# Kernel tuning notes

Measured on AMD Instinct MI355X. Metric: run time of the kernel, lower is better.

## Reference

```python
import jax, jax.numpy as jnp
import numpy as np

B, T, C = 4, 2048, 1024
HEAD = 64  # n_embd // n_heads


def setup_inputs() -> dict:
    key = jax.random.key(0)
    kx, kk, kq, kv = jax.random.split(key, 4)
    x = jax.random.normal(kx, (B, T, C), dtype=jnp.float32)
    # nn.Linear(n_embd, head_size, bias=False) weights have shape [head_size, n_embd]
    s = 1.0 / np.sqrt(C)
    Wk = jax.random.normal(kk, (HEAD, C), dtype=jnp.float32) * s
    Wq = jax.random.normal(kq, (HEAD, C), dtype=jnp.float32) * s
    Wv = jax.random.normal(kv, (HEAD, C), dtype=jnp.float32) * s
    return {"x": x, "Wk": Wk, "Wq": Wq, "Wv": Wv}


def reference(x, Wk, Wq, Wv):
    Bx, Tx, Cx = x.shape
    k = jnp.einsum("btc,hc->bth", x, Wk)  # [B,T,HEAD]
    q = jnp.einsum("btc,hc->bth", x, Wq)
    v = jnp.einsum("btc,hc->bth", x, Wv)
    # NOTE: original scales by C**-0.5 (C = n_embd), not head_size**-0.5
    scale = Cx ** (-0.5)
    wei = jnp.einsum("bth,bsh->bts", q, k) * scale  # [B,T,T]
    causal = jnp.tril(jnp.ones((Tx, Tx), dtype=bool))
    wei = jnp.where(causal, wei, -jnp.inf)
    wei = jax.nn.softmax(wei, axis=-1)
    # dropout p=0.0 (eval) -> identity
    out = jnp.einsum("bts,bsh->bth", wei, v)  # [B,T,HEAD]
    return out
```

## Files before the change

kernel.cpp:

```cpp
#include <hip/hip_runtime.h>
#include <math.h>

#define Tn 2048
#define Cn 1024
#define Hn 64

using u16 = unsigned short;
typedef float f32x4 __attribute__((ext_vector_type(4)));
typedef __bf16 bf16x8 __attribute__((ext_vector_type(8)));
typedef u16 u16x8 __attribute__((ext_vector_type(8)));
typedef u16 u16x4 __attribute__((ext_vector_type(4)));

__device__ __forceinline__ u16 f2bf(float f) {
    return __builtin_bit_cast(u16, static_cast<__bf16>(f));
}

__global__ __launch_bounds__(256) void wpack_kernel(
    const float* __restrict__ Wk, const float* __restrict__ Wq,
    const float* __restrict__ Wv, u16* __restrict__ wp)
{
    int slot = blockIdx.x * 256 + threadIdx.x;
    int n16  = slot >> 11;
    int rem  = slot & 2047;
    int kc   = rem >> 6;
    int lane = rem & 63;
    int l15 = lane & 15, lg = lane >> 4;
    int col = n16 * 16 + l15;
    const float* __restrict__ Wm = (col < 64) ? Wk : (col < 128) ? Wq : Wv;
    float sc = (col >= 64 && col < 128) ? 0.03125f : 1.0f;
    const float* src = &Wm[(size_t)(col & 63) * Cn + kc * 32 + lg * 8];
    float4 lo = *reinterpret_cast<const float4*>(src);
    float4 hi = *reinterpret_cast<const float4*>(src + 4);
    u16x8 o;
    o[0] = f2bf(lo.x * sc); o[1] = f2bf(lo.y * sc);
    o[2] = f2bf(lo.z * sc); o[3] = f2bf(lo.w * sc);
    o[4] = f2bf(hi.x * sc); o[5] = f2bf(hi.y * sc);
    o[6] = f2bf(hi.z * sc); o[7] = f2bf(hi.w * sc);
    *reinterpret_cast<u16x8*>(&wp[(size_t)slot * 8]) = o;
}

__global__ __launch_bounds__(512) void qkv_proj(
    const float* __restrict__ x, const u16* __restrict__ wp,
    u16* __restrict__ kb, u16* __restrict__ qb, u16* __restrict__ vb)
{
    __shared__ float xs[2][32 * 68];

    const int tid  = threadIdx.x;
    const int lane = tid & 63;
    const int w    = tid >> 6;
    const int rg   = w & 1;
    const int cg   = w >> 1;
    const int l15  = lane & 15;
    const int lg   = lane >> 4;

    const int row0 = blockIdx.x * 32;
    const int sr   = tid >> 4;
    const int scc  = (tid & 15) << 2;

    f32x4 acc[3];
#pragma unroll
    for (int nt = 0; nt < 3; ++nt)
#pragma unroll
        for (int r = 0; r < 4; ++r) acc[nt][r] = 0.f;

    const float* __restrict__ xsrc = &x[(size_t)(row0 + sr) * Cn + scc];

    float4 g = *reinterpret_cast<const float4*>(xsrc);
    *reinterpret_cast<float4*>(&xs[0][sr * 68 + scc]) = g;
    __syncthreads();

    for (int ks = 0; ks < 16; ++ks) {
        const int cur = ks & 1;
        if (ks < 15)
            g = *reinterpret_cast<const float4*>(xsrc + (ks + 1) * 64);
#pragma unroll
        for (int kc2 = 0; kc2 < 2; ++kc2) {
            const float* ap = &xs[cur][(rg * 16 + l15) * 68 + kc2 * 32 + (lg << 3)];
            f32x4 a0 = *reinterpret_cast<const f32x4*>(ap);
            f32x4 a1 = *reinterpret_cast<const f32x4*>(ap + 4);
            bf16x8 a;
            a[0] = (__bf16)a0[0]; a[1] = (__bf16)a0[1];
            a[2] = (__bf16)a0[2]; a[3] = (__bf16)a0[3];
            a[4] = (__bf16)a1[0]; a[5] = (__bf16)a1[1];
            a[6] = (__bf16)a1[2]; a[7] = (__bf16)a1[3];
            const int kcg = ks * 2 + kc2;
#pragma unroll
            for (int nt = 0; nt < 3; ++nt) {
                const int n16 = cg * 3 + nt;
                bf16x8 bfr = *reinterpret_cast<const bf16x8*>(
                    &wp[(size_t)((n16 * 32 + kcg) * 64 + lane) * 8]);
                acc[nt] = __builtin_amdgcn_mfma_f32_16x16x32_bf16(a, bfr, acc[nt], 0, 0, 0);
            }
        }
        if (ks < 15)
            *reinterpret_cast<float4*>(&xs[cur ^ 1][sr * 68 + scc]) = g;
        __syncthreads();
    }

#pragma unroll
    for (int nt = 0; nt < 3; ++nt) {
        const int n16  = cg * 3 + nt;
        const int col0 = n16 * 16;
        const int mat  = col0 >> 6;
        u16* __restrict__ ob = (mat == 0) ? kb : (mat == 1) ? qb : vb;
        const int h = (col0 & 63) + l15;
#pragma unroll
        for (int reg = 0; reg < 4; ++reg) {
            const int grow = row0 + rg * 16 + (lg << 2) + reg;
            ob[(size_t)grow * Hn + h] = f2bf(acc[nt][reg]);
        }
    }
}

__global__ __launch_bounds__(256) void attn(
    const u16* __restrict__ qb, const u16* __restrict__ kb,
    const u16* __restrict__ vb, float* __restrict__ Opart,
    float* __restrict__ mlb)
{
    __shared__ u16 Ks[2][64 * 72];
    __shared__ u16 VTs[2][64 * 72];
    __shared__ u16 Pl[4][16 * 72];

    const int tid  = threadIdx.x;
    const int lane = tid & 63;
    const int w    = tid >> 6;
    const int g    = w >> 1;
    const int p    = w & 1;
    const int l15  = lane & 15;
    const int lg   = lane >> 4;

    const int bid = blockIdx.x;
    const int b = bid / 288;
    const int r = bid % 288;
    int gq = (int)((sqrtf((float)r + 1.0f) - 1.0f) * 0.5f);
    while (4 * (gq + 1) * (gq + 2) <= r) ++gq;
    while (4 * gq * (gq + 1) > r) --gq;
    const int rr = r - 4 * gq * (gq + 1);
    const int qt = gq * 8 + rr / (gq + 1);
    const int c  = rr % (gq + 1);

    const int t0  = qt * 32;
    const int wr0 = t0 + g * 16;
    const int nkt = ((t0 + 31) >> 6) + 1;
    const size_t kvbase = (size_t)b * Tn * Hn;

    bf16x8 qf[2];
    {
        const u16* qrow = qb + ((size_t)(b * Tn + wr0 + l15)) * Hn;
        qf[0] = *reinterpret_cast<const bf16x8*>(&qrow[(lg << 3)]);
        qf[1] = *reinterpret_cast<const bf16x8*>(&qrow[32 + (lg << 3)]);
    }

    f32x4 o[4];
    float m[4], ls[4];
#pragma unroll
    for (int nt = 0; nt < 4; ++nt)
#pragma unroll
        for (int rg2 = 0; rg2 < 4; ++rg2) o[nt][rg2] = 0.f;
#pragma unroll
    for (int rg2 = 0; rg2 < 4; ++rg2) { m[rg2] = -INFINITY; ls[rg2] = 0.f; }

    for (int s = 0; s < 2; ++s) {
        const int kt0 = c * 4 + 2 * s, kt1 = kt0 + 1;
        if (kt0 < nkt) {
#pragma unroll
            for (int i = 0; i < 2; ++i) {
                int cc = tid + 256 * i;
                int rr2 = cc >> 3, c8 = (cc & 7) << 3;
                *reinterpret_cast<u16x8*>(&Ks[0][rr2 * 72 + c8]) =
                    *reinterpret_cast<const u16x8*>(&kb[kvbase + (size_t)(kt0 * 64 + rr2) * Hn + c8]);
            }
#pragma unroll
            for (int i = 0; i < 2; ++i) {
                int cc = tid + 256 * i;
                int k = cc & 63, d0 = (cc >> 6) << 3;
                u16x8 v = *reinterpret_cast<const u16x8*>(&vb[kvbase + (size_t)(kt0 * 64 + k) * Hn + d0]);
#pragma unroll
                for (int j = 0; j < 8; ++j) VTs[0][(d0 + j) * 72 + k] = v[j];
            }
        }
        if (kt1 < nkt) {
#pragma unroll
            for (int i = 0; i < 2; ++i) {
                int cc = tid + 256 * i;
                int rr2 = cc >> 3, c8 = (cc & 7) << 3;
                *reinterpret_cast<u16x8*>(&Ks[1][rr2 * 72 + c8]) =
                    *reinterpret_cast<const u16x8*>(&kb[kvbase + (size_t)(kt1 * 64 + rr2) * Hn + c8]);
            }
#pragma unroll
            for (int i = 0; i < 2; ++i) {
                int cc = tid + 256 * i;
                int k = cc & 63, d0 = (cc >> 6) << 3;
                u16x8 v = *reinterpret_cast<const u16x8*>(&vb[kvbase + (size_t)(kt1 * 64 + k) * Hn + d0]);
#pragma unroll
                for (int j = 0; j < 8; ++j) VTs[1][(d0 + j) * 72 + k] = v[j];
            }
        }
        __syncthreads();

        const int mykt = kt0 + p;
        if (mykt < nkt) {
            f32x4 sf[4];
#pragma unroll
            for (int nt = 0; nt < 4; ++nt)
#pragma unroll
                for (int rg2 = 0; rg2 < 4; ++rg2) sf[nt][rg2] = 0.f;
            __builtin_amdgcn_s_setprio(1);
#pragma unroll
            for (int kc = 0; kc < 2; ++kc) {
#pragma unroll
                for (int nt = 0; nt < 4; ++nt) {
                    bf16x8 kf = *reinterpret_cast<const bf16x8*>(
                        &Ks[p][(nt * 16 + l15) * 72 + kc * 32 + (lg << 3)]);
                    sf[nt] = __builtin_amdgcn_mfma_f32_16x16x32_bf16(qf[kc], kf, sf[nt], 0, 0, 0);
                }
            }
            __builtin_amdgcn_s_setprio(0);
            if (mykt * 64 + 63 > wr0) {
#pragma unroll
                for (int nt = 0; nt < 4; ++nt) {
                    int kg = mykt * 64 + nt * 16 + l15;
#pragma unroll
                    for (int reg = 0; reg < 4; ++reg) {
                        int tq = wr0 + (lg << 2) + reg;
                        if (kg > tq) sf[nt][reg] = -INFINITY;
                    }
                }
            }
            float tm[4];
            bool defok = true;
#pragma unroll
            for (int reg = 0; reg < 4; ++reg) {
                float t = fmaxf(fmaxf(sf[0][reg], sf[1][reg]),
                                fmaxf(sf[2][reg], sf[3][reg]));
#pragma unroll
                for (int off = 1; off < 16; off <<= 1)
                    t = fmaxf(t, __shfl_xor(t, off, 64));
                tm[reg] = t;
                defok = defok && (t <= m[reg] + 8.f);
            }
            if (!__all(defok ? 1 : 0)) {
#pragma unroll
                for (int reg = 0; reg < 4; ++reg) {
                    float nm = fmaxf(m[reg], tm[reg]);
                    float al = __expf(m[reg] - nm);
                    ls[reg] *= al;
#pragma unroll
                    for (int nt = 0; nt < 4; ++nt) o[nt][reg] *= al;
                    m[reg] = nm;
                }
            }
            float pv[4][4];
#pragma unroll
            for (int reg = 0; reg < 4; ++reg) {
                float rs = 0.f;
#pragma unroll
                for (int nt = 0; nt < 4; ++nt) {
                    pv[nt][reg] = __expf(sf[nt][reg] - m[reg]);
                    rs += pv[nt][reg];
                }
#pragma unroll
                for (int off = 1; off < 16; off <<= 1)
                    rs += __shfl_xor(rs, off, 64);
                ls[reg] += rs;
            }
#pragma unroll
            for (int nt = 0; nt < 4; ++nt)
#pragma unroll
                for (int reg = 0; reg < 4; ++reg)
                    Pl[w][((lg << 2) + reg) * 72 + nt * 16 + l15] = f2bf(pv[nt][reg]);
#pragma unroll
            for (int kc = 0; kc < 2; ++kc) {
                bf16x8 pa = *reinterpret_cast<const bf16x8*>(
                    &Pl[w][l15 * 72 + kc * 32 + (lg << 3)]);
                __builtin_amdgcn_s_setprio(1);
#pragma unroll
                for (int nt = 0; nt < 4; ++nt) {
                    bf16x8 vf = *reinterpret_cast<const bf16x8*>(
                        &VTs[p][(nt * 16 + l15) * 72 + kc * 32 + (lg << 3)]);
                    o[nt] = __builtin_amdgcn_mfma_f32_16x16x32_bf16(pa, vf, o[nt], 0, 0, 0);
                }
                __builtin_amdgcn_s_setprio(0);
            }
        }
        __syncthreads();
    }

    float* slab = reinterpret_cast<float*>(&Ks[0][0]);
    float* sb = slab + g * (24 * 64);
    if (p == 1) {
#pragma unroll
        for (int nt = 0; nt < 4; ++nt)
#pragma unroll
            for (int reg = 0; reg < 4; ++reg)
                sb[(nt * 4 + reg) * 64 + lane] = o[nt][reg];
#pragma unroll
        for (int reg = 0; reg < 4; ++reg) {
            sb[(16 + reg) * 64 + lane] = m[reg];
            sb[(20 + reg) * 64 + lane] = ls[reg];
        }
    }
    __syncthreads();
    if (p == 0) {
        const size_t pidx = (size_t)(b * 64 + qt) * 8 + c;
        float* __restrict__ ob = Opart + pidx * 2048;
#pragma unroll
        for (int reg = 0; reg < 4; ++reg) {
            float mB = sb[(16 + reg) * 64 + lane];
            float lB = sb[(20 + reg) * 64 + lane];
            float ms = fmaxf(m[reg], mB);
            float aA = __expf(m[reg] - ms);
            float aB = __expf(mB - ms);
            int row32 = g * 16 + (lg << 2) + reg;
            if (l15 == 0) {
                float* mlp = mlb + pidx * 64 + row32 * 2;
                mlp[0] = ms;
                mlp[1] = aA * ls[reg] + aB * lB;
            }
#pragma unroll
            for (int nt = 0; nt < 4; ++nt)
                ob[row32 * 64 + nt * 16 + l15] =
                    aA * o[nt][reg] + aB * sb[(nt * 4 + reg) * 64 + lane];
        }
    }
}

__global__ __launch_bounds__(256) void attn_merge(
    const float* __restrict__ Opart, const float* __restrict__ mlb,
    float* __restrict__ out)
{
    const int bid = blockIdx.x;
    const int b = bid >> 6, qt = bid & 63;
    const int nch = (qt >> 3) + 1;
    const int t = threadIdx.x;
    const int row = t >> 3, d0 = (t & 7) << 3;
    const size_t pbase = (size_t)(b * 64 + qt) * 8;

    float mc[8], lc[8];
#pragma unroll
    for (int cc = 0; cc < 8; ++cc) {
        if (cc < nch) {
            const float* mlp = mlb + (pbase + cc) * 64 + row * 2;
            mc[cc] = mlp[0];
            lc[cc] = mlp[1];
        } else { mc[cc] = -INFINITY; lc[cc] = 0.f; }
    }
    float mfin = mc[0];
#pragma unroll
    for (int cc = 1; cc < 8; ++cc) mfin = fmaxf(mfin, mc[cc]);

    float wgt[8], l = 0.f;
#pragma unroll
    for (int cc = 0; cc < 8; ++cc) {
        wgt[cc] = (cc < nch) ? __expf(mc[cc] - mfin) : 0.f;
        l += lc[cc] * wgt[cc];
    }

    f32x4 O0 = {0.f, 0.f, 0.f, 0.f}, O1 = {0.f, 0.f, 0.f, 0.f};
#pragma unroll
    for (int cc = 0; cc < 8; ++cc) {
        if (cc < nch) {
            const float* op = Opart + (pbase + cc) * 2048 + row * 64 + d0;
            f32x4 c0 = *reinterpret_cast<const f32x4*>(op);
            f32x4 c1 = *reinterpret_cast<const f32x4*>(op + 4);
            O0 += c0 * wgt[cc];
            O1 += c1 * wgt[cc];
        }
    }
    float inv = 1.f / l;
    float* orow = out + ((size_t)(b * Tn + qt * 32 + row)) * Hn + d0;
    *reinterpret_cast<f32x4*>(orow)     = O0 * inv;
    *reinterpret_cast<f32x4*>(orow + 4) = O1 * inv;
}

extern "C" void kernel_launch(void* const* d_in, const int* in_sizes, int n_in,
                              void* d_out, int out_size, void* d_ws, size_t ws_size,
                              hipStream_t stream) {
    const float* x  = (const float*)d_in[0];
    const float* Wk = (const float*)d_in[1];
    const float* Wq = (const float*)d_in[2];
    const float* Wv = (const float*)d_in[3];
    float* out = (float*)d_out;

    const size_t rows = (size_t)4 * Tn;
    u16* kbuf = (u16*)d_ws;
    u16* qbuf = kbuf + rows * Hn;
    u16* vbuf = qbuf + rows * Hn;
    u16* wpk  = vbuf + rows * Hn;
    float* Opart = (float*)(wpk + 196608);
    float* mlb   = Opart + (size_t)4 * 64 * 8 * 2048;

    wpack_kernel<<<96, 256, 0, stream>>>(Wk, Wq, Wv, wpk);
    qkv_proj<<<256, 512, 0, stream>>>(x, wpk, kbuf, qbuf, vbuf);
    attn<<<1152, 256, 0, stream>>>(qbuf, kbuf, vbuf, Opart, mlb);
    attn_merge<<<256, 256, 0, stream>>>(Opart, mlb, out);
}
```

Baseline: 49.22 us.

## Use larger KV chunks per block and write unsplit rows directly to output

Changes the split-KV decomposition so each attention block processes up to 8 KV tiles (4 rounds) instead of 4. This reduces the block count from 1152 to 640 and the number of partial chunks per query tile from up to 8 to up to 4. Query tiles with a single chunk (the first 16) now normalize and write straight to the output, so the merge kernel only handles the remaining 48 tiles per batch. The s_setprio hints around the MFMA loops are removed. The trade-off is fewer, longer blocks and therefore less parallelism and coarser load balance, in exchange for less partial-output traffic and merge work.

```diff
diff --git a/kernel.cpp b/kernel.cpp
--- a/kernel.cpp
+++ b/kernel.cpp
@@ -115,7 +115,7 @@
 __global__ __launch_bounds__(256) void attn(
     const u16* __restrict__ qb, const u16* __restrict__ kb,
     const u16* __restrict__ vb, float* __restrict__ Opart,
-    float* __restrict__ mlb)
+    float* __restrict__ mlb, float* __restrict__ out)
 {
     __shared__ u16 Ks[2][64 * 72];
     __shared__ u16 VTs[2][64 * 72];
@@ -130,18 +130,19 @@
     const int lg   = lane >> 4;
 
     const int bid = blockIdx.x;
-    const int b = bid / 288;
-    const int r = bid % 288;
-    int gq = (int)((sqrtf((float)r + 1.0f) - 1.0f) * 0.5f);
-    while (4 * (gq + 1) * (gq + 2) <= r) ++gq;
-    while (4 * gq * (gq + 1) > r) --gq;
-    const int rr = r - 4 * gq * (gq + 1);
-    const int qt = gq * 8 + rr / (gq + 1);
+    const int b = bid / 160;
+    const int r = bid % 160;
+    int gq = 3;
+    while (8 * gq * (gq + 1) > r) --gq;
+    const int rr = r - 8 * gq * (gq + 1);
+    const int qt = gq * 16 + rr / (gq + 1);
     const int c  = rr % (gq + 1);
+    const int c8 = c * 8;
 
     const int t0  = qt * 32;
     const int wr0 = t0 + g * 16;
-    const int nkt = ((t0 + 31) >> 6) + 1;
+    const int nkt = (qt >> 1) + 1;
+    const int rounds = (nkt - c8 + 1) >> 1 < 4 ? (nkt - c8 + 1) >> 1 : 4;
     const size_t kvbase = (size_t)b * Tn * Hn;
 
     bf16x8 qf[2];
@@ -160,15 +161,15 @@
 #pragma unroll
     for (int rg2 = 0; rg2 < 4; ++rg2) { m[rg2] = -INFINITY; ls[rg2] = 0.f; }
 
-    for (int s = 0; s < 2; ++s) {
-        const int kt0 = c * 4 + 2 * s, kt1 = kt0 + 1;
-        if (kt0 < nkt) {
+    for (int s = 0; s < rounds; ++s) {
+        const int kt0 = c8 + 2 * s, kt1 = kt0 + 1;
+        {
 #pragma unroll
             for (int i = 0; i < 2; ++i) {
                 int cc = tid + 256 * i;
-                int rr2 = cc >> 3, c8 = (cc & 7) << 3;
-                *reinterpret_cast<u16x8*>(&Ks[0][rr2 * 72 + c8]) =
-                    *reinterpret_cast<const u16x8*>(&kb[kvbase + (size_t)(kt0 * 64 + rr2) * Hn + c8]);
+                int rr2 = cc >> 3, cb = (cc & 7) << 3;
+                *reinterpret_cast<u16x8*>(&Ks[0][rr2 * 72 + cb]) =
+                    *reinterpret_cast<const u16x8*>(&kb[kvbase + (size_t)(kt0 * 64 + rr2) * Hn + cb]);
             }
 #pragma unroll
             for (int i = 0; i < 2; ++i) {
@@ -183,9 +184,9 @@
 #pragma unroll
             for (int i = 0; i < 2; ++i) {
                 int cc = tid + 256 * i;
-                int rr2 = cc >> 3, c8 = (cc & 7) << 3;
-                *reinterpret_cast<u16x8*>(&Ks[1][rr2 * 72 + c8]) =
-                    *reinterpret_cast<const u16x8*>(&kb[kvbase + (size_t)(kt1 * 64 + rr2) * Hn + c8]);
+                int rr2 = cc >> 3, cb = (cc & 7) << 3;
+                *reinterpret_cast<u16x8*>(&Ks[1][rr2 * 72 + cb]) =
+                    *reinterpret_cast<const u16x8*>(&kb[kvbase + (size_t)(kt1 * 64 + rr2) * Hn + cb]);
             }
 #pragma unroll
             for (int i = 0; i < 2; ++i) {
@@ -205,7 +206,6 @@
             for (int nt = 0; nt < 4; ++nt)
 #pragma unroll
                 for (int rg2 = 0; rg2 < 4; ++rg2) sf[nt][rg2] = 0.f;
-            __builtin_amdgcn_s_setprio(1);
 #pragma unroll
             for (int kc = 0; kc < 2; ++kc) {
 #pragma unroll
@@ -215,7 +215,6 @@
                     sf[nt] = __builtin_amdgcn_mfma_f32_16x16x32_bf16(qf[kc], kf, sf[nt], 0, 0, 0);
                 }
             }
-            __builtin_amdgcn_s_setprio(0);
             if (mykt * 64 + 63 > wr0) {
 #pragma unroll
                 for (int nt = 0; nt < 4; ++nt) {
@@ -273,14 +272,12 @@
             for (int kc = 0; kc < 2; ++kc) {
                 bf16x8 pa = *reinterpret_cast<const bf16x8*>(
                     &Pl[w][l15 * 72 + kc * 32 + (lg << 3)]);
-                __builtin_amdgcn_s_setprio(1);
 #pragma unroll
                 for (int nt = 0; nt < 4; ++nt) {
                     bf16x8 vf = *reinterpret_cast<const bf16x8*>(
                         &VTs[p][(nt * 16 + l15) * 72 + kc * 32 + (lg << 3)]);
                     o[nt] = __builtin_amdgcn_mfma_f32_16x16x32_bf16(pa, vf, o[nt], 0, 0, 0);
                 }
-                __builtin_amdgcn_s_setprio(0);
             }
         }
         __syncthreads();
@@ -302,25 +299,43 @@
     }
     __syncthreads();
     if (p == 0) {
-        const size_t pidx = (size_t)(b * 64 + qt) * 8 + c;
-        float* __restrict__ ob = Opart + pidx * 2048;
-#pragma unroll
-        for (int reg = 0; reg < 4; ++reg) {
-            float mB = sb[(16 + reg) * 64 + lane];
-            float lB = sb[(20 + reg) * 64 + lane];
-            float ms = fmaxf(m[reg], mB);
-            float aA = __expf(m[reg] - ms);
-            float aB = __expf(mB - ms);
-            int row32 = g * 16 + (lg << 2) + reg;
-            if (l15 == 0) {
-                float* mlp = mlb + pidx * 64 + row32 * 2;
-                mlp[0] = ms;
-                mlp[1] = aA * ls[reg] + aB * lB;
-            }
-#pragma unroll
-            for (int nt = 0; nt < 4; ++nt)
-                ob[row32 * 64 + nt * 16 + l15] =
-                    aA * o[nt][reg] + aB * sb[(nt * 4 + reg) * 64 + lane];
+        if (gq == 0) {
+#pragma unroll
+            for (int reg = 0; reg < 4; ++reg) {
+                float mB = sb[(16 + reg) * 64 + lane];
+                float lB = sb[(20 + reg) * 64 + lane];
+                float ms = fmaxf(m[reg], mB);
+                float aA = __expf(m[reg] - ms);
+                float aB = __expf(mB - ms);
+                float inv = 1.0f / (aA * ls[reg] + aB * lB);
+                int grow = t0 + g * 16 + (lg << 2) + reg;
+                float* orow = out + ((size_t)(b * Tn) + grow) * Hn;
+#pragma unroll
+                for (int nt = 0; nt < 4; ++nt)
+                    orow[nt * 16 + l15] =
+                        (aA * o[nt][reg] + aB * sb[(nt * 4 + reg) * 64 + lane]) * inv;
+            }
+        } else {
+            const size_t pidx = (size_t)(b * 64 + qt) * 4 + c;
+            float* __restrict__ ob = Opart + pidx * 2048;
+#pragma unroll
+            for (int reg = 0; reg < 4; ++reg) {
+                float mB = sb[(16 + reg) * 64 + lane];
+                float lB = sb[(20 + reg) * 64 + lane];
+                float ms = fmaxf(m[reg], mB);
+                float aA = __expf(m[reg] - ms);
+                float aB = __expf(mB - ms);
+                int row32 = g * 16 + (lg << 2) + reg;
+                if (l15 == 0) {
+                    float* mlp = mlb + pidx * 64 + row32 * 2;
+                    mlp[0] = ms;
+                    mlp[1] = aA * ls[reg] + aB * lB;
+                }
+#pragma unroll
+                for (int nt = 0; nt < 4; ++nt)
+                    ob[row32 * 64 + nt * 16 + l15] =
+                        aA * o[nt][reg] + aB * sb[(nt * 4 + reg) * 64 + lane];
+            }
         }
     }
 }
@@ -330,35 +345,34 @@
     float* __restrict__ out)
 {
     const int bid = blockIdx.x;
-    const int b = bid >> 6, qt = bid & 63;
-    const int nch = (qt >> 3) + 1;
+    const int b  = bid / 48;
+    const int qt = 16 + bid % 48;
+    const int nch = (qt >> 4) + 1;
     const int t = threadIdx.x;
     const int row = t >> 3, d0 = (t & 7) << 3;
-    const size_t pbase = (size_t)(b * 64 + qt) * 8;
-
-    float mc[8], lc[8];
-#pragma unroll
-    for (int cc = 0; cc < 8; ++cc) {
+    const size_t pbase = (size_t)(b * 64 + qt) * 4;
+
+    float mc[4], lc[4];
+#pragma unroll
+    for (int cc = 0; cc < 4; ++cc) {
         if (cc < nch) {
             const float* mlp = mlb + (pbase + cc) * 64 + row * 2;
             mc[cc] = mlp[0];
             lc[cc] = mlp[1];
         } else { mc[cc] = -INFINITY; lc[cc] = 0.f; }
     }
-    float mfin = mc[0];
-#pragma unroll
-    for (int cc = 1; cc < 8; ++cc) mfin = fmaxf(mfin, mc[cc]);
-
-    float wgt[8], l = 0.f;
-#pragma unroll
-    for (int cc = 0; cc < 8; ++cc) {
+    float mfin = fmaxf(fmaxf(mc[0], mc[1]), fmaxf(mc[2], mc[3]));
+
+    float wgt[4], l = 0.f;
+#pragma unroll
+    for (int cc = 0; cc < 4; ++cc) {
         wgt[cc] = (cc < nch) ? __expf(mc[cc] - mfin) : 0.f;
         l += lc[cc] * wgt[cc];
     }
 
     f32x4 O0 = {0.f, 0.f, 0.f, 0.f}, O1 = {0.f, 0.f, 0.f, 0.f};
 #pragma unroll
-    for (int cc = 0; cc < 8; ++cc) {
+    for (int cc = 0; cc < 4; ++cc) {
         if (cc < nch) {
             const float* op = Opart + (pbase + cc) * 2048 + row * 64 + d0;
             f32x4 c0 = *reinterpret_cast<const f32x4*>(op);
@@ -388,10 +402,10 @@
     u16* vbuf = qbuf + rows * Hn;
     u16* wpk  = vbuf + rows * Hn;
     float* Opart = (float*)(wpk + 196608);
-    float* mlb   = Opart + (size_t)4 * 64 * 8 * 2048;
+    float* mlb   = Opart + (size_t)256 * 4 * 2048;
 
     wpack_kernel<<<96, 256, 0, stream>>>(Wk, Wq, Wv, wpk);
     qkv_proj<<<256, 512, 0, stream>>>(x, wpk, kbuf, qbuf, vbuf);
-    attn<<<1152, 256, 0, stream>>>(qbuf, kbuf, vbuf, Opart, mlb);
-    attn_merge<<<256, 256, 0, stream>>>(Opart, mlb, out);
-}
+    attn<<<640, 256, 0, stream>>>(qbuf, kbuf, vbuf, Opart, mlb, out);
+    attn_merge<<<192, 256, 0, stream>>>(Opart, mlb, out);
+}
```

After: 46.60 us. 1.06x faster.
